# Optimization experiments

Hardware: AMD Instinct MI355X
Metric: run time of the kernel (lower is better)

Reference implementation:

```python
import jax, jax.numpy as jnp
import numpy as np

B, C = 2048, 512          # batch, channels
CHG = 16                  # coarse grid side (16x16 -> N=256)
FHG = 16                  # fine grid side (16x16 -> F=256)
N = CHG * CHG             # coarse_span.total
F = FHG * FHG             # fine_total
K = 4                     # top4 sample mode
LOG_F = float(np.log(F))


def _ln(x, g, b, eps=1e-5):
    m = jnp.mean(x, axis=-1, keepdims=True)
    v = jnp.var(x, axis=-1, keepdims=True)
    return (x - m) * jax.lax.rsqrt(v + eps) * g + b


def _mlp3(x, w1, b1, w2, b2, w3, b3):
    # linear_stack: Linear+gelu, Linear+gelu, Linear (dropout=0 / eval)
    h = jax.nn.gelu(x @ w1 + b1)
    h = jax.nn.gelu(h @ w2 + b2)
    return h @ w3 + b3


def setup_inputs() -> dict:
    key = jax.random.key(0)
    ks = jax.random.split(key, 10)
    s = 0.02
    return {
        'x': jax.random.normal(ks[0], (B, C), jnp.float32),
        'in_g': jnp.ones((C,), jnp.float32), 'in_b': jnp.zeros((C,), jnp.float32),
        'nop_w': jax.random.normal(ks[1], (C, 1), jnp.float32) * s,
        'nop_b': jnp.zeros((1,), jnp.float32),
        'c_w1': jax.random.normal(ks[2], (C, C), jnp.float32) * s,
        'c_b1': jnp.zeros((C,), jnp.float32),
        'c_w2': jax.random.normal(ks[3], (C, C), jnp.float32) * s,
        'c_b2': jnp.zeros((C,), jnp.float32),
        'c_w3': jax.random.normal(ks[4], (C, N), jnp.float32) * s,
        'c_b3': jnp.zeros((N,), jnp.float32),
        'emb': jax.random.normal(ks[5], (N, C), jnp.float32),
        'emb_g': jnp.ones((C,), jnp.float32), 'emb_b': jnp.zeros((C,), jnp.float32),
        'f_w1': jax.random.normal(ks[6], (2 * C, C), jnp.float32) * s,
        'f_b1': jnp.zeros((C,), jnp.float32),
        'f_w2': jax.random.normal(ks[7], (C, C), jnp.float32) * s,
        'f_b2': jnp.zeros((C,), jnp.float32),
        'f_w3': jax.random.normal(ks[8], (C, F), jnp.float32) * s,
        'f_b3': jnp.zeros((F,), jnp.float32),
    }


def reference(x, in_g, in_b, nop_w, nop_b, c_w1, c_b1, c_w2, c_b2, c_w3, c_b3,
              emb, emb_g, emb_b, f_w1, f_b1, f_w2, f_b2, f_w3, f_b3):
    xn = _ln(x, in_g, in_b)                                  # (B,C)
    no_op = xn @ nop_w + nop_b                               # (B,1)
    coarse = _mlp3(xn, c_w1, c_b1, c_w2, c_b2, c_w3, c_b3)   # (B,N)
    _, idx = jax.lax.top_k(coarse, K)                        # (B,K) int32
    e = _ln(emb[idx], emb_g, emb_b)                          # (B,K,C)
    fin = jnp.concatenate([jnp.broadcast_to(xn[:, None, :], (B, K, C)), e], axis=-1)
    fine = _mlp3(fin, f_w1, f_b1, f_w2, f_b2, f_w3, f_b3)    # (B,K,F)
    # scatter value: coarse[b,i] - log F + fine + log F - lse(fine) = coarse[b,i] + log_softmax(fine)
    vals = jnp.take_along_axis(coarse, idx, axis=1)[:, :, None] + jax.nn.log_softmax(fine, axis=-1)
    dense = jnp.broadcast_to((coarse - LOG_F)[:, :, None], (B, N, F))
    dense = dense.at[jnp.arange(B)[:, None], idx].set(vals)  # top-k indices are distinct
    # view (B, ch0, ch1, fh0, fh1) -> permute (0,1,3,2,4) -> flatten
    xname = dense.reshape(B, CHG, CHG, FHG, FHG).transpose(0, 1, 3, 2, 4).reshape(B, -1)
    return jnp.concatenate([no_op, xname], axis=-1)          # (B, 1 + N*F)
```

## Files before the change

kernel.cpp:

```cpp
#include <hip/hip_runtime.h>
#include <math.h>

#define BATCH 2048
#define CH 512
#define N_COARSE 256
#define F_FINE 256
#define K_TOP 4
#define OUT_STRIDE 65537

typedef unsigned short ushort_t;
typedef __bf16 bf16x8 __attribute__((ext_vector_type(8)));
typedef float f32x4 __attribute__((ext_vector_type(4)));

typedef __attribute__((address_space(3))) unsigned int lds_uint;
typedef __attribute__((address_space(1))) unsigned int gl_uint;

__device__ __forceinline__ void gload_lds16(const ushort_t* g, ushort_t* l) {
    __builtin_amdgcn_global_load_lds((const gl_uint*)g, (lds_uint*)l, 16, 0, 0);
}

__device__ __forceinline__ float gelu_tanh(float x) {
    float x3 = x * x * x;
    float t = tanhf(0.7978845608028654f * (x + 0.044715f * x3));
    return 0.5f * x * (1.0f + t);
}

__device__ __forceinline__ ushort_t f2bf(float f) {
    unsigned u = __float_as_uint(f);
    unsigned r = (u + 0x7FFF + ((u >> 16) & 1)) >> 16;
    return (ushort_t)r;
}
__device__ __forceinline__ float bf2f(ushort_t h) {
    return __uint_as_float(((unsigned)h) << 16);
}

struct Params {
    const float *x, *in_g, *in_b, *nop_w, *nop_b;
    const float *c_w1, *c_b1, *c_w2, *c_b2, *c_w3, *c_b3;
    const float *emb, *emb_g, *emb_b;
    const float *f_w1, *f_b1, *f_w2, *f_b2, *f_w3, *f_b3;
    float *coarse, *fine, *out, *cvals;
    ushort_t *xnsp, *h1sp, *h2sp, *e_bf, *fh1_bf, *fh2_bf;
    ushort_t *wt1, *wt2, *wt3, *cwt1, *cwt2, *cwt3;
    int *idxb;
};

__global__ __launch_bounds__(256) void prep_kernel(Params p) {
    __shared__ float s[32][33];
    int u = blockIdx.x, t = threadIdx.x;
    if (u < 1536) {
        const float* W; ushort_t* Wt; int Kd, Nd, gx, gy; bool split;
        if (u < 512)       { W=p.f_w1; Wt=p.wt1; Kd=1024; Nd=512; gx=u&15; gy=u>>4; split=false; }
        else if (u < 768)  { int v=u-512;  W=p.f_w2; Wt=p.wt2; Kd=512; Nd=512; gx=v&15; gy=v>>4; split=false; }
        else if (u < 896)  { int v=u-768;  W=p.f_w3; Wt=p.wt3; Kd=512; Nd=256; gx=v&7;  gy=v>>3; split=false; }
        else if (u < 1152) { int v=u-896;  W=p.c_w1; Wt=p.cwt1; Kd=512; Nd=512; gx=v&15; gy=v>>4; split=true; }
        else if (u < 1408) { int v=u-1152; W=p.c_w2; Wt=p.cwt2; Kd=512; Nd=512; gx=v&15; gy=v>>4; split=true; }
        else               { int v=u-1408; W=p.c_w3; Wt=p.cwt3; Kd=512; Nd=256; gx=v&7;  gy=v>>3; split=true; }
        int tx = t & 31, ty = t >> 5;
        int n0 = gx * 32, k0 = gy * 32;
        #pragma unroll
        for (int i = 0; i < 4; ++i) {
            int r = ty + i * 8;
            s[r][tx] = W[(size_t)(k0 + r) * Nd + n0 + tx];
        }
        __syncthreads();
        if (!split) {
            #pragma unroll
            for (int i = 0; i < 4; ++i) {
                int r = ty + i * 8;
                Wt[(size_t)(n0 + r) * Kd + k0 + tx] = f2bf(s[tx][r]);
            }
        } else {
            #pragma unroll
            for (int i = 0; i < 4; ++i) {
                int r = ty + i * 8;
                float v = s[tx][r];
                ushort_t h = f2bf(v);
                Wt[(size_t)(n0 + r) * 1024 + k0 + tx] = h;
                Wt[(size_t)(n0 + r) * 1024 + 512 + k0 + tx] = f2bf(v - bf2f(h));
            }
        }
    } else {
        float* red = &s[0][0];
        int row = u - 1536;
        int lane = t & 63, wave = t >> 6;
        const float* xr = p.x + (size_t)row * CH;
        float v0 = xr[t], v1 = xr[t + 256];
        float sm = v0 + v1, ss = v0 * v0 + v1 * v1;
        #pragma unroll
        for (int off = 32; off; off >>= 1) { sm += __shfl_xor(sm, off); ss += __shfl_xor(ss, off); }
        if (lane == 0) { red[wave] = sm; red[4 + wave] = ss; }
        __syncthreads();
        sm = red[0] + red[1] + red[2] + red[3];
        ss = red[4] + red[5] + red[6] + red[7];
        float mean = sm * (1.0f / CH);
        float var = ss * (1.0f / CH) - mean * mean;
        float rsq = rsqrtf(var + 1e-5f);
        float xn0 = (v0 - mean) * rsq * p.in_g[t] + p.in_b[t];
        float xn1 = (v1 - mean) * rsq * p.in_g[t + 256] + p.in_b[t + 256];
        ushort_t* xr2 = p.xnsp + (size_t)row * 1024;
        ushort_t h0 = f2bf(xn0), h1v = f2bf(xn1);
        xr2[t] = h0; xr2[t + 256] = h1v;
        xr2[512 + t] = f2bf(xn0 - bf2f(h0));
        xr2[512 + t + 256] = f2bf(xn1 - bf2f(h1v));
        float d = xn0 * p.nop_w[t] + xn1 * p.nop_w[t + 256];
        #pragma unroll
        for (int off = 32; off; off >>= 1) d += __shfl_xor(d, off);
        __syncthreads();
        if (lane == 0) red[wave] = d;
        __syncthreads();
        if (t == 0) p.out[(size_t)row * OUT_STRIDE] = red[0] + red[1] + red[2] + red[3] + p.nop_b[0];
    }
}

template<int MODE, int MT, int NT, int OUTM>
__global__ __launch_bounds__(256) void mfma_gemm_kernel(
    const ushort_t* __restrict__ A1, const ushort_t* __restrict__ A2,
    const ushort_t* __restrict__ Wt, const float* __restrict__ bias,
    const float* __restrict__ cvals, void* __restrict__ Cout, int Nd, int Ktot)
{
    constexpr int FI = MT / 32, FJ = NT / 32;
    __shared__ ushort_t As[2][MT * 32];
    __shared__ ushort_t Bs[2][NT * 32];
    __shared__ float mxs[64 * 2];
    __shared__ float ses[64 * 2];
    int t = threadIdx.x;
    int n0 = blockIdx.x * NT, m0 = blockIdx.y * MT;
    int wave = t >> 6, lane = t & 63;
    int wm = (wave & 1) * (MT / 2), wn = (wave >> 1) * (NT / 2);
    int lr = lane & 15, quad = lane >> 4;
    int wbase = wave * 64;

    f32x4 acc[FI][FJ] = {};

    auto stageAB = [&](int k0, int pp) {
        int aoff = (MODE == 2) ? ((k0 >= 1024) ? k0 - 512 : (k0 & 511)) : k0;
        int woff = (MODE == 2) ? ((k0 >= 1024) ? k0 - 1024 : k0) : k0;
        constexpr int AL = MT * 4;
        constexpr int BL = NT * 4;
        if constexpr (AL >= 256) {
            #pragma unroll
            for (int i = 0; i < AL / 256; ++i) {
                int c = i * 256 + t, r = c >> 2, q = (c & 3) * 8;
                int gr = m0 + r;
                const ushort_t* ap;
                if (MODE == 1)      ap = (k0 < 512) ? A1 + (size_t)(gr >> 2) * 1024 + k0 + q
                                                    : A2 + (size_t)gr * 512 + (k0 - 512) + q;
                else if (MODE == 2) ap = A1 + (size_t)gr * 1024 + aoff + q;
                else                ap = A1 + (size_t)gr * Ktot + k0 + q;
                gload_lds16(ap, &As[pp][(i * 256 + wbase) * 8]);
            }
        } else {
            if (t < AL) {
                int c = t, r = c >> 2, q = (c & 3) * 8;
                int gr = m0 + r;
                const ushort_t* ap;
                if (MODE == 1)      ap = (k0 < 512) ? A1 + (size_t)(gr >> 2) * 1024 + k0 + q
                                                    : A2 + (size_t)gr * 512 + (k0 - 512) + q;
                else if (MODE == 2) ap = A1 + (size_t)gr * 1024 + aoff + q;
                else                ap = A1 + (size_t)gr * Ktot + k0 + q;
                gload_lds16(ap, &As[pp][wbase * 8]);
            }
        }
        if constexpr (BL >= 256) {
            #pragma unroll
            for (int i = 0; i < BL / 256; ++i) {
                int c = i * 256 + t, r = c >> 2, q = (c & 3) * 8;
                size_t wstride = (MODE == 2) ? 1024 : (size_t)Ktot;
                const ushort_t* bp = Wt + (size_t)(n0 + r) * wstride + woff + q;
                gload_lds16(bp, &Bs[pp][(i * 256 + wbase) * 8]);
            }
        } else {
            if (t < BL) {
                int c = t, r = c >> 2, q = (c & 3) * 8;
                size_t wstride = (MODE == 2) ? 1024 : (size_t)Ktot;
                const ushort_t* bp = Wt + (size_t)(n0 + r) * wstride + woff + q;
                gload_lds16(bp, &Bs[pp][wbase * 8]);
            }
        }
    };

    stageAB(0, 0);
    int steps = Ktot >> 5;
    int p = 0;
    for (int s = 0; s < steps; ++s) {
        __syncthreads();
        if (s + 1 < steps) stageAB((s + 1) * 32, p ^ 1);
        bf16x8 af[FI], bfr[FJ];
        #pragma unroll
        for (int i = 0; i < FI; ++i)
            af[i] = *(const bf16x8*)&As[p][(wm + i * 16 + lr) * 32 + quad * 8];
        #pragma unroll
        for (int j = 0; j < FJ; ++j)
            bfr[j] = *(const bf16x8*)&Bs[p][(wn + j * 16 + lr) * 32 + quad * 8];
        #pragma unroll
        for (int i = 0; i < FI; ++i)
            #pragma unroll
            for (int j = 0; j < FJ; ++j)
                acc[i][j] = __builtin_amdgcn_mfma_f32_16x16x32_bf16(af[i], bfr[j], acc[i][j], 0, 0, 0);
        p ^= 1;
    }

    if (OUTM == 3) {
        float bv[FJ];
        #pragma unroll
        for (int j = 0; j < FJ; ++j) bv[j] = bias[wn + j * 16 + lr];
        int half = wave >> 1;
        float rmx[FI][4];
        #pragma unroll
        for (int i = 0; i < FI; ++i)
            #pragma unroll
            for (int r = 0; r < 4; ++r) {
                float m = -1e30f;
                #pragma unroll
                for (int j = 0; j < FJ; ++j) m = fmaxf(m, acc[i][j][r] + bv[j]);
                #pragma unroll
                for (int mk = 1; mk < 16; mk <<= 1) m = fmaxf(m, __shfl_xor(m, mk));
                if (lr == 0) mxs[(wm + i * 16 + quad * 4 + r) * 2 + half] = m;
            }
        __syncthreads();
        #pragma unroll
        for (int i = 0; i < FI; ++i)
            #pragma unroll
            for (int r = 0; r < 4; ++r) {
                int rl = wm + i * 16 + quad * 4 + r;
                rmx[i][r] = fmaxf(mxs[rl * 2], mxs[rl * 2 + 1]);
            }
        #pragma unroll
        for (int i = 0; i < FI; ++i)
            #pragma unroll
            for (int r = 0; r < 4; ++r) {
                float sv = 0.f;
                #pragma unroll
                for (int j = 0; j < FJ; ++j) sv += expf(acc[i][j][r] + bv[j] - rmx[i][r]);
                #pragma unroll
                for (int mk = 1; mk < 16; mk <<= 1) sv += __shfl_xor(sv, mk);
                if (lr == 0) ses[(wm + i * 16 + quad * 4 + r) * 2 + half] = sv;
            }
        __syncthreads();
        float* outp = (float*)Cout;
        #pragma unroll
        for (int i = 0; i < FI; ++i)
            #pragma unroll
            for (int r = 0; r < 4; ++r) {
                int rl = wm + i * 16 + quad * 4 + r;
                float se = ses[rl * 2] + ses[rl * 2 + 1];
                float addc = cvals[m0 + rl] - rmx[i][r] - logf(se);
                #pragma unroll
                for (int j = 0; j < FJ; ++j)
                    outp[(size_t)(m0 + rl) * Nd + wn + j * 16 + lr] = acc[i][j][r] + bv[j] + addc;
            }
    } else {
        #pragma unroll
        for (int j = 0; j < FJ; ++j) {
            int col = n0 + wn + j * 16 + lr;
            float bvv = bias[col];
            #pragma unroll
            for (int i = 0; i < FI; ++i) {
                #pragma unroll
                for (int r = 0; r < 4; ++r) {
                    int row = m0 + wm + i * 16 + quad * 4 + r;
                    float val = acc[i][j][r] + bvv;
                    if (OUTM == 0) {
                        ((ushort_t*)Cout)[(size_t)row * Nd + col] = f2bf(gelu_tanh(val));
                    } else if (OUTM == 1) {
                        float gv = gelu_tanh(val);
                        ushort_t h = f2bf(gv);
                        ((ushort_t*)Cout)[(size_t)row * 1024 + col] = h;
                        ((ushort_t*)Cout)[(size_t)row * 1024 + 512 + col] = f2bf(gv - bf2f(h));
                    } else {
                        ((float*)Cout)[(size_t)row * Nd + col] = val;
                    }
                }
            }
        }
    }
}

__global__ __launch_bounds__(256) void topk_embln_kernel(Params p) {
    __shared__ int sidx[4];
    int brow = blockIdx.x, t = threadIdx.x;
    int wave = t >> 6, lane = t & 63;
    if (wave == 0) {
        const float* cr = p.coarse + (size_t)brow * N_COARSE;
        float v[4]; int id[4];
        #pragma unroll
        for (int j = 0; j < 4; ++j) { v[j] = cr[lane + 64 * j]; id[j] = lane + 64 * j; }
        #pragma unroll
        for (int r = 0; r < K_TOP; ++r) {
            float bv = v[0]; int bi = id[0];
            #pragma unroll
            for (int j = 1; j < 4; ++j)
                if (v[j] > bv || (v[j] == bv && id[j] < bi)) { bv = v[j]; bi = id[j]; }
            #pragma unroll
            for (int off = 32; off; off >>= 1) {
                float ov = __shfl_xor(bv, off); int oi = __shfl_xor(bi, off);
                if (ov > bv || (ov == bv && oi < bi)) { bv = ov; bi = oi; }
            }
            if ((bi & 63) == lane) v[bi >> 6] = -INFINITY;
            if (lane == 0) {
                sidx[r] = bi;
                p.idxb[brow * K_TOP + r] = bi;
                p.cvals[brow * K_TOP + r] = bv;
            }
        }
    }
    __syncthreads();
    int n = sidx[wave];
    const float* er = p.emb + (size_t)n * CH + lane * 8;
    float4 u0 = *(const float4*)er;
    float4 u1 = *(const float4*)(er + 4);
    float s  = u0.x + u0.y + u0.z + u0.w + u1.x + u1.y + u1.z + u1.w;
    float ss = u0.x * u0.x + u0.y * u0.y + u0.z * u0.z + u0.w * u0.w
             + u1.x * u1.x + u1.y * u1.y + u1.z * u1.z + u1.w * u1.w;
    #pragma unroll
    for (int off = 32; off; off >>= 1) { s += __shfl_xor(s, off); ss += __shfl_xor(ss, off); }
    float mean = s * (1.0f / CH);
    float var = ss * (1.0f / CH) - mean * mean;
    float rsq = rsqrtf(var + 1e-5f);
    float4 g0 = *(const float4*)(p.emb_g + lane * 8), g1 = *(const float4*)(p.emb_g + lane * 8 + 4);
    float4 b0 = *(const float4*)(p.emb_b + lane * 8), b1 = *(const float4*)(p.emb_b + lane * 8 + 4);
    uint4 pk;
    pk.x = (unsigned)f2bf((u0.x - mean) * rsq * g0.x + b0.x) |
           ((unsigned)f2bf((u0.y - mean) * rsq * g0.y + b0.y) << 16);
    pk.y = (unsigned)f2bf((u0.z - mean) * rsq * g0.z + b0.z) |
           ((unsigned)f2bf((u0.w - mean) * rsq * g0.w + b0.w) << 16);
    pk.z = (unsigned)f2bf((u1.x - mean) * rsq * g1.x + b1.x) |
           ((unsigned)f2bf((u1.y - mean) * rsq * g1.y + b1.y) << 16);
    pk.w = (unsigned)f2bf((u1.z - mean) * rsq * g1.z + b1.z) |
           ((unsigned)f2bf((u1.w - mean) * rsq * g1.w + b1.w) << 16);
    *(uint4*)(p.e_bf + (size_t)(brow * K_TOP + wave) * CH + lane * 8) = pk;
}

__global__ __launch_bounds__(256) void scatter_kernel(Params p) {
    const float LOG_F = 5.545177444479562f;
    int b = blockIdx.y, cx = blockIdx.x, t = threadIdx.x;
    int4 ii = *(const int4*)&p.idxb[b * 4];
    size_t rowb = (size_t)b * OUT_STRIDE + 1;
    #pragma unroll
    for (int q = 0; q < 4; ++q) {
        int o = cx * 4096 + q * 1024 + t * 4;
        int c0 = o >> 12, f0 = (o >> 8) & 15, c1 = (o >> 4) & 15, f1 = o & 15;
        int n = c0 * 16 + c1;
        int f = f0 * 16 + f1;
        int k = -1;
        if (n == ii.x) k = 0; else if (n == ii.y) k = 1; else if (n == ii.z) k = 2; else if (n == ii.w) k = 3;
        float r0, r1, r2, r3;
        if (k >= 0) {
            float4 u = *(const float4*)(p.fine + ((size_t)(b * 4 + k)) * F_FINE + f);
            r0 = u.x; r1 = u.y; r2 = u.z; r3 = u.w;
        } else {
            float base = p.coarse[(size_t)b * N_COARSE + n] - LOG_F;
            r0 = r1 = r2 = r3 = base;
        }
        float* op = p.out + rowb + o;
        __builtin_nontemporal_store(r0, op + 0);
        __builtin_nontemporal_store(r1, op + 1);
        __builtin_nontemporal_store(r2, op + 2);
        __builtin_nontemporal_store(r3, op + 3);
    }
}

extern "C" void kernel_launch(void* const* d_in, const int* in_sizes, int n_in,
                              void* d_out, int out_size, void* d_ws, size_t ws_size,
                              hipStream_t stream) {
    Params prm;
    prm.x     = (const float*)d_in[0];
    prm.in_g  = (const float*)d_in[1];
    prm.in_b  = (const float*)d_in[2];
    prm.nop_w = (const float*)d_in[3];
    prm.nop_b = (const float*)d_in[4];
    prm.c_w1  = (const float*)d_in[5];
    prm.c_b1  = (const float*)d_in[6];
    prm.c_w2  = (const float*)d_in[7];
    prm.c_b2  = (const float*)d_in[8];
    prm.c_w3  = (const float*)d_in[9];
    prm.c_b3  = (const float*)d_in[10];
    prm.emb   = (const float*)d_in[11];
    prm.emb_g = (const float*)d_in[12];
    prm.emb_b = (const float*)d_in[13];
    prm.f_w1  = (const float*)d_in[14];
    prm.f_b1  = (const float*)d_in[15];
    prm.f_w2  = (const float*)d_in[16];
    prm.f_b2  = (const float*)d_in[17];
    prm.f_w3  = (const float*)d_in[18];
    prm.f_b3  = (const float*)d_in[19];

    float* ws = (float*)d_ws;
    prm.coarse  = ws;
    prm.fine    = prm.coarse + 524288;
    prm.xnsp    = (ushort_t*)(prm.fine + 2097152);
    prm.h1sp    = prm.xnsp + 2097152;
    prm.h2sp    = prm.h1sp + 2097152;
    prm.e_bf    = prm.h2sp + 2097152;
    prm.fh1_bf  = prm.e_bf + 4194304;
    prm.fh2_bf  = prm.fh1_bf + 4194304;
    prm.wt1     = prm.fh2_bf + 4194304;
    prm.wt2     = prm.wt1 + 524288;
    prm.wt3     = prm.wt2 + 262144;
    prm.cwt1    = prm.wt3 + 131072;
    prm.cwt2    = prm.cwt1 + 524288;
    prm.cwt3    = prm.cwt2 + 524288;
    prm.idxb    = (int*)(prm.cwt3 + 262144);
    prm.cvals   = (float*)(prm.idxb + 8192);
    prm.out     = (float*)d_out;

    prep_kernel<<<3584, 256, 0, stream>>>(prm);
    mfma_gemm_kernel<2, 32, 64, 1><<<dim3(8, 64), 256, 0, stream>>>(
        prm.xnsp, nullptr, prm.cwt1, prm.c_b1, nullptr, prm.h1sp, 512, 1536);
    mfma_gemm_kernel<2, 32, 64, 1><<<dim3(8, 64), 256, 0, stream>>>(
        prm.h1sp, nullptr, prm.cwt2, prm.c_b2, nullptr, prm.h2sp, 512, 1536);
    mfma_gemm_kernel<2, 32, 32, 2><<<dim3(8, 64), 256, 0, stream>>>(
        prm.h2sp, nullptr, prm.cwt3, prm.c_b3, nullptr, prm.coarse, 256, 1536);
    topk_embln_kernel<<<BATCH, 256, 0, stream>>>(prm);
    mfma_gemm_kernel<1, 64, 64, 0><<<dim3(8, 128), 256, 0, stream>>>(
        prm.xnsp, prm.e_bf, prm.wt1, prm.f_b1, nullptr, prm.fh1_bf, 512, 1024);
    mfma_gemm_kernel<0, 64, 64, 0><<<dim3(8, 128), 256, 0, stream>>>(
        prm.fh1_bf, nullptr, prm.wt2, prm.f_b2, nullptr, prm.fh2_bf, 512, 512);
    mfma_gemm_kernel<0, 32, 256, 3><<<dim3(1, 256), 256, 0, stream>>>(
        prm.fh2_bf, nullptr, prm.wt3, prm.f_b3, prm.cvals, prm.fine, 256, 512);
    scatter_kernel<<<dim3(16, BATCH), 256, 0, stream>>>(prm);
}
```

Baseline: 720.1 us.

## Fuse background scatter into fine-MLP GEMM launches and write fine outputs directly

Removes the standalone scatter kernel. The background fill (coarse minus log F), which skips the top-k slots, is now spread as extra blocks across the three fine-MLP GEMM grids, so those memory-bound stores can overlap with GEMM compute. The final log-softmax GEMM epilogue writes its values straight into their permuted positions in the output instead of staging them in a fine buffer. This saves the intermediate buffer and one launch, at the cost of extra grid blocks per GEMM, strided nontemporal stores from the epilogue, and a hand-coded split of scatter units across launches.

```diff
diff --git a/kernel.cpp b/kernel.cpp
--- a/kernel.cpp
+++ b/kernel.cpp
@@ -39,7 +39,7 @@
     const float *c_w1, *c_b1, *c_w2, *c_b2, *c_w3, *c_b3;
     const float *emb, *emb_g, *emb_b;
     const float *f_w1, *f_b1, *f_w2, *f_b2, *f_w3, *f_b3;
-    float *coarse, *fine, *out, *cvals;
+    float *coarse, *out, *cvals;
     ushort_t *xnsp, *h1sp, *h2sp, *e_bf, *fh1_bf, *fh2_bf;
     ushort_t *wt1, *wt2, *wt3, *cwt1, *cwt2, *cwt3;
     int *idxb;
@@ -113,12 +113,43 @@
     }
 }
 
+__device__ __forceinline__ void bg_scatter_unit(const float* __restrict__ coarse,
+                                                const int* __restrict__ idxb,
+                                                float* __restrict__ out, int gu) {
+    const float LOG_F = 5.545177444479562f;
+    int b = gu >> 4, cx = gu & 15, t = threadIdx.x;
+    int4 ii = *(const int4*)&idxb[b * 4];
+    size_t rowb = (size_t)b * OUT_STRIDE + 1;
+    const float* cr = coarse + (size_t)b * N_COARSE;
+    #pragma unroll
+    for (int q = 0; q < 4; ++q) {
+        int o = cx * 4096 + q * 1024 + t * 4;
+        int n = ((o >> 12) << 4) | ((o >> 4) & 15);
+        bool skip = (n == ii.x) | (n == ii.y) | (n == ii.z) | (n == ii.w);
+        if (!skip) {
+            float base = cr[n] - LOG_F;
+            float* op = out + rowb + o;
+            __builtin_nontemporal_store(base, op + 0);
+            __builtin_nontemporal_store(base, op + 1);
+            __builtin_nontemporal_store(base, op + 2);
+            __builtin_nontemporal_store(base, op + 3);
+        }
+    }
+}
+
 template<int MODE, int MT, int NT, int OUTM>
 __global__ __launch_bounds__(256) void mfma_gemm_kernel(
     const ushort_t* __restrict__ A1, const ushort_t* __restrict__ A2,
     const ushort_t* __restrict__ Wt, const float* __restrict__ bias,
-    const float* __restrict__ cvals, void* __restrict__ Cout, int Nd, int Ktot)
+    const float* __restrict__ cvals, void* __restrict__ Cout, int Nd, int Ktot,
+    const float* __restrict__ coarseB, const int* __restrict__ idxbB,
+    float* __restrict__ outB, int gemmY, int suBase)
 {
+    if ((int)blockIdx.y >= gemmY) {
+        int gu = suBase + ((int)blockIdx.y - gemmY) * (int)gridDim.x + (int)blockIdx.x;
+        bg_scatter_unit(coarseB, idxbB, outB, gu);
+        return;
+    }
     constexpr int FI = MT / 32, FJ = NT / 32;
     __shared__ ushort_t As[2][MT * 32];
     __shared__ ushort_t Bs[2][NT * 32];
@@ -238,7 +269,6 @@
                 if (lr == 0) ses[(wm + i * 16 + quad * 4 + r) * 2 + half] = sv;
             }
         __syncthreads();
-        float* outp = (float*)Cout;
         #pragma unroll
         for (int i = 0; i < FI; ++i)
             #pragma unroll
@@ -246,9 +276,14 @@
                 int rl = wm + i * 16 + quad * 4 + r;
                 float se = ses[rl * 2] + ses[rl * 2 + 1];
                 float addc = cvals[m0 + rl] - rmx[i][r] - logf(se);
+                int m = m0 + rl;
+                int n = idxbB[m];
+                size_t base = (size_t)(m >> 2) * OUT_STRIDE + 1
+                            + (size_t)((n >> 4) * 4096 + (n & 15) * 16);
                 #pragma unroll
                 for (int j = 0; j < FJ; ++j)
-                    outp[(size_t)(m0 + rl) * Nd + wn + j * 16 + lr] = acc[i][j][r] + bv[j] + addc;
+                    __builtin_nontemporal_store(acc[i][j][r] + bv[j] + addc,
+                        &outB[base + (size_t)((wn >> 4) + j) * 256 + lr]);
             }
     } else {
         #pragma unroll
@@ -332,35 +367,6 @@
     *(uint4*)(p.e_bf + (size_t)(brow * K_TOP + wave) * CH + lane * 8) = pk;
 }
 
-__global__ __launch_bounds__(256) void scatter_kernel(Params p) {
-    const float LOG_F = 5.545177444479562f;
-    int b = blockIdx.y, cx = blockIdx.x, t = threadIdx.x;
-    int4 ii = *(const int4*)&p.idxb[b * 4];
-    size_t rowb = (size_t)b * OUT_STRIDE + 1;
-    #pragma unroll
-    for (int q = 0; q < 4; ++q) {
-        int o = cx * 4096 + q * 1024 + t * 4;
-        int c0 = o >> 12, f0 = (o >> 8) & 15, c1 = (o >> 4) & 15, f1 = o & 15;
-        int n = c0 * 16 + c1;
-        int f = f0 * 16 + f1;
-        int k = -1;
-        if (n == ii.x) k = 0; else if (n == ii.y) k = 1; else if (n == ii.z) k = 2; else if (n == ii.w) k = 3;
-        float r0, r1, r2, r3;
-        if (k >= 0) {
-            float4 u = *(const float4*)(p.fine + ((size_t)(b * 4 + k)) * F_FINE + f);
-            r0 = u.x; r1 = u.y; r2 = u.z; r3 = u.w;
-        } else {
-            float base = p.coarse[(size_t)b * N_COARSE + n] - LOG_F;
-            r0 = r1 = r2 = r3 = base;
-        }
-        float* op = p.out + rowb + o;
-        __builtin_nontemporal_store(r0, op + 0);
-        __builtin_nontemporal_store(r1, op + 1);
-        __builtin_nontemporal_store(r2, op + 2);
-        __builtin_nontemporal_store(r3, op + 3);
-    }
-}
-
 extern "C" void kernel_launch(void* const* d_in, const int* in_sizes, int n_in,
                               void* d_out, int out_size, void* d_ws, size_t ws_size,
                               hipStream_t stream) {
@@ -388,8 +394,7 @@
 
     float* ws = (float*)d_ws;
     prm.coarse  = ws;
-    prm.fine    = prm.coarse + 524288;
-    prm.xnsp    = (ushort_t*)(prm.fine + 2097152);
+    prm.xnsp    = (ushort_t*)(prm.coarse + 524288);
     prm.h1sp    = prm.xnsp + 2097152;
     prm.h2sp    = prm.h1sp + 2097152;
     prm.e_bf    = prm.h2sp + 2097152;
@@ -405,19 +410,26 @@
     prm.cvals   = (float*)(prm.idxb + 8192);
     prm.out     = (float*)d_out;
 
+    const int NOSC = 1 << 28;
+
     prep_kernel<<<3584, 256, 0, stream>>>(prm);
     mfma_gemm_kernel<2, 32, 64, 1><<<dim3(8, 64), 256, 0, stream>>>(
-        prm.xnsp, nullptr, prm.cwt1, prm.c_b1, nullptr, prm.h1sp, 512, 1536);
+        prm.xnsp, nullptr, prm.cwt1, prm.c_b1, nullptr, prm.h1sp, 512, 1536,
+        nullptr, nullptr, nullptr, NOSC, 0);
     mfma_gemm_kernel<2, 32, 64, 1><<<dim3(8, 64), 256, 0, stream>>>(
-        prm.h1sp, nullptr, prm.cwt2, prm.c_b2, nullptr, prm.h2sp, 512, 1536);
+        prm.h1sp, nullptr, prm.cwt2, prm.c_b2, nullptr, prm.h2sp, 512, 1536,
+        nullptr, nullptr, nullptr, NOSC, 0);
     mfma_gemm_kernel<2, 32, 32, 2><<<dim3(8, 64), 256, 0, stream>>>(
-        prm.h2sp, nullptr, prm.cwt3, prm.c_b3, nullptr, prm.coarse, 256, 1536);
+        prm.h2sp, nullptr, prm.cwt3, prm.c_b3, nullptr, prm.coarse, 256, 1536,
+        nullptr, nullptr, nullptr, NOSC, 0);
     topk_embln_kernel<<<BATCH, 256, 0, stream>>>(prm);
-    mfma_gemm_kernel<1, 64, 64, 0><<<dim3(8, 128), 256, 0, stream>>>(
-        prm.xnsp, prm.e_bf, prm.wt1, prm.f_b1, nullptr, prm.fh1_bf, 512, 1024);
-    mfma_gemm_kernel<0, 64, 64, 0><<<dim3(8, 128), 256, 0, stream>>>(
-        prm.fh1_bf, nullptr, prm.wt2, prm.f_b2, nullptr, prm.fh2_bf, 512, 512);
-    mfma_gemm_kernel<0, 32, 256, 3><<<dim3(1, 256), 256, 0, stream>>>(
-        prm.fh2_bf, nullptr, prm.wt3, prm.f_b3, prm.cvals, prm.fine, 256, 512);
-    scatter_kernel<<<dim3(16, BATCH), 256, 0, stream>>>(prm);
-}
+    mfma_gemm_kernel<1, 64, 64, 0><<<dim3(8, 128 + 1364), 256, 0, stream>>>(
+        prm.xnsp, prm.e_bf, prm.wt1, prm.f_b1, nullptr, prm.fh1_bf, 512, 1024,
+        prm.coarse, prm.idxb, prm.out, 128, 0);
+    mfma_gemm_kernel<0, 64, 64, 0><<<dim3(8, 128 + 1364), 256, 0, stream>>>(
+        prm.fh1_bf, nullptr, prm.wt2, prm.f_b2, nullptr, prm.fh2_bf, 512, 512,
+        prm.coarse, prm.idxb, prm.out, 128, 10912);
+    mfma_gemm_kernel<0, 32, 256, 3><<<dim3(1, 256 + 10944), 256, 0, stream>>>(
+        prm.fh2_bf, nullptr, prm.wt3, prm.f_b3, prm.cvals, nullptr, 256, 512,
+        prm.coarse, prm.idxb, prm.out, 256, 21824);
+}
```

Measured after the change: 683.1 us. -5.1%, faster.
